# Kernel tuning notes

Measured on AMD Instinct MI355X. Metric: run time of the kernel, lower is better.

The kernel has to match this reference:

```python
import jax, jax.numpy as jnp
import numpy as np

B, S, D = 4, 4096, 2048
DFF = 4 * D
SKIP = 0.125


def setup_inputs() -> dict:
    key = jax.random.key(0)
    ks = jax.random.split(key, 4)
    s_in = 1.0 / np.sqrt(D).astype(np.float32)
    s_ff = 1.0 / np.sqrt(DFF).astype(np.float32)
    return {
        "x": jax.random.normal(ks[0], (B, S, D), jnp.float32),
        "Wr": jax.random.normal(ks[1], (D, 1), jnp.float32) * s_in,
        "br": jnp.zeros((1,), jnp.float32),
        "W1": jax.random.normal(ks[2], (D, DFF), jnp.float32) * s_in,
        "b1": jnp.zeros((DFF,), jnp.float32),
        "W2": jax.random.normal(ks[3], (DFF, D), jnp.float32) * s_ff,
        "b2": jnp.zeros((D,), jnp.float32),
    }


def reference(x, Wr, br, W1, b1, W2, b2):
    Bs, Ss, Ds = x.shape
    k = max(int(Ss * SKIP), 1)
    # Router: tiny linear D -> 1
    logits = (x @ Wr + br)[..., 0]                      # [B, S]
    # Top-k token selection along sequence
    weights, idx = jax.lax.top_k(logits, k)             # [B, k] (unsorted order within topk)
    perm = jnp.argsort(idx, axis=1)                     # torch.sort's sort-indices
    tokens = jnp.take_along_axis(idx, perm, axis=1)     # sorted token positions [B, k]
    # Gather selected tokens
    fx = jnp.take_along_axis(x, tokens[..., None], axis=1)  # [B, k, D]
    h = jax.nn.gelu(fx @ W1 + b1, approximate=False)    # [B, k, 4D]
    out_l = h @ W2 + b2                                  # [B, k, D]
    # Softmax over topk router logits, reordered to sorted-token order
    tw = jax.nn.softmax(weights, axis=1)                # [B, k]
    rw = jnp.take_along_axis(tw, perm, axis=1)          # [B, k]
    xw = rw[..., None] * out_l                           # [B, k, D]
    # scatter_add back onto x at the selected token positions
    bidx = jnp.arange(Bs)[:, None]                       # [B, 1]
    return x.at[bidx, tokens].add(xw)
```

## Files before the change

### kernel.cpp

```cpp
#include <hip/hip_runtime.h>
#include <math.h>

#define B_DIM   4
#define S_DIM   4096
#define D_DIM   2048
#define DFF_DIM 8192
#define K_TOP   512
#define M_ROWS  (B_DIM * K_TOP)
#define NSPLIT  4

typedef _Float16 half8 __attribute__((ext_vector_type(8)));
typedef _Float16 half4 __attribute__((ext_vector_type(4)));
typedef float    floatx4 __attribute__((ext_vector_type(4)));

static const size_t OFF_LOGITS = 0;
static const size_t OFF_SELMAP = 0;
static const size_t OFF_TOK    = 65536;
static const size_t OFF_RW     = 73728;
static const size_t OFF_FX     = 81920;
static const size_t OFF_W1T    = OFF_FX  + (size_t)M_ROWS * D_DIM * 2;
static const size_t OFF_W2T    = OFF_W1T + (size_t)DFF_DIM * D_DIM * 2;
static const size_t OFF_H      = OFF_W2T + (size_t)D_DIM * DFF_DIM * 2;
static const size_t WS_NEEDED  = OFF_H   + (size_t)M_ROWS * DFF_DIM * 2;
static const size_t OFF_PART   = OFF_W1T;

__device__ __forceinline__ void async_ld16(const void* g, void* l) {
  __builtin_amdgcn_global_load_lds((const __attribute__((address_space(1))) unsigned int*)g,
                                   (__attribute__((address_space(3))) unsigned int*)l,
                                   16, 0, 0);
}

#define WAITCNT_VM0   0x0F70
#define WAITCNT_LGKM0 0xC07F

__global__ __launch_bounds__(256) void router_logits(const float* __restrict__ x,
                                                     const float* __restrict__ Wr,
                                                     const float* __restrict__ br,
                                                     float* __restrict__ logits) {
  int row  = blockIdx.x * 4 + (threadIdx.x >> 6);
  int lane = threadIdx.x & 63;
  const float4* xr = (const float4*)(x + (size_t)row * D_DIM);
  const float4* wr = (const float4*)Wr;
  float s = 0.f;
#pragma unroll
  for (int i = 0; i < (D_DIM / 4) / 64; ++i) {
    float4 a = xr[lane + i * 64];
    float4 w = wr[lane + i * 64];
    s += a.x * w.x + a.y * w.y + a.z * w.z + a.w * w.w;
  }
#pragma unroll
  for (int off = 32; off > 0; off >>= 1) s += __shfl_down(s, off, 64);
  if (lane == 0) logits[row] = s + br[0];
}

__global__ __launch_bounds__(256) void topk_select(const float* logits,
                                                   int* selmap,
                                                   int* __restrict__ tokens,
                                                   float* __restrict__ rw) {
  int b = blockIdx.x;
  const float* lg = logits + (size_t)b * S_DIM;
  __shared__ unsigned int keys[S_DIM];
  __shared__ unsigned int bins[256];
  __shared__ unsigned int sscan[256];
  __shared__ unsigned int sh_prefix, sh_r;
  __shared__ float sel_logit[K_TOP];
  __shared__ float red[8];

  int tid = threadIdx.x;
  for (int s = tid; s < S_DIM; s += 256) {
    unsigned int u = __float_as_uint(lg[s]);
    keys[s] = (u & 0x80000000u) ? ~u : (u | 0x80000000u);
    selmap[b * S_DIM + s] = -1;
  }
  if (tid == 0) { sh_prefix = 0u; sh_r = K_TOP; }
  __syncthreads();

  for (int p = 24; p >= 0; p -= 8) {
    bins[tid] = 0u;
    __syncthreads();
    unsigned int prefix = sh_prefix;
    unsigned int maskhi = (p == 24) ? 0u : (0xFFFFFFFFu << (p + 8));
    for (int s = tid; s < S_DIM; s += 256) {
      unsigned int kk = keys[s];
      if ((kk & maskhi) == prefix) atomicAdd(&bins[(kk >> p) & 255u], 1u);
    }
    __syncthreads();
    sscan[tid] = bins[255 - tid];
    __syncthreads();
#pragma unroll
    for (int off = 1; off < 256; off <<= 1) {
      unsigned int v = (tid >= off) ? sscan[tid - off] : 0u;
      __syncthreads();
      sscan[tid] += v;
      __syncthreads();
    }
    unsigned int r = sh_r;
    unsigned int above = (tid > 0) ? sscan[tid - 1] : 0u;
    bool hit = (sscan[tid] >= r) && (above < r);
    __syncthreads();
    if (hit) {
      sh_prefix = prefix | ((unsigned int)(255 - tid) << p);
      sh_r = r - above;
    }
    __syncthreads();
  }
  unsigned int T = sh_prefix;

  int s0 = tid * 16;
  unsigned int g = 0, e = 0;
#pragma unroll
  for (int j = 0; j < 16; ++j) {
    unsigned int kk = keys[s0 + j];
    g += (kk > T);
    e += (kk == T);
  }
  sscan[tid] = g | (e << 16);
  __syncthreads();
#pragma unroll
  for (int off = 1; off < 256; off <<= 1) {
    unsigned int v = (tid >= off) ? sscan[tid - off] : 0u;
    __syncthreads();
    sscan[tid] += v;
    __syncthreads();
  }
  unsigned int incl = sscan[tid];
  unsigned int Gtot = sscan[255] & 0xFFFFu;
  unsigned int need = (unsigned int)K_TOP - Gtot;
  unsigned int gr = (incl & 0xFFFFu) - g;
  unsigned int er = (incl >> 16) - e;
#pragma unroll
  for (int j = 0; j < 16; ++j) {
    unsigned int kk = keys[s0 + j];
    if (kk > T) {
      unsigned int pos = gr + (er < need ? er : need);
      tokens[b * K_TOP + (int)pos] = s0 + j;
      sel_logit[pos] = __uint_as_float((kk & 0x80000000u) ? (kk & 0x7FFFFFFFu) : ~kk);
      selmap[b * S_DIM + s0 + j] = (int)pos;
      gr++;
    } else if (kk == T) {
      if (er < need) {
        unsigned int pos = gr + er;
        tokens[b * K_TOP + (int)pos] = s0 + j;
        sel_logit[pos] = __uint_as_float((kk & 0x80000000u) ? (kk & 0x7FFFFFFFu) : ~kk);
        selmap[b * S_DIM + s0 + j] = (int)pos;
      }
      er++;
    }
  }
  __syncthreads();

  int lane = tid & 63, wv = tid >> 6;
  float mx = -1e30f;
  for (int i = tid; i < K_TOP; i += 256) mx = fmaxf(mx, sel_logit[i]);
#pragma unroll
  for (int off = 32; off > 0; off >>= 1) mx = fmaxf(mx, __shfl_down(mx, off, 64));
  if (lane == 0) red[wv] = mx;
  __syncthreads();
  if (tid == 0) red[0] = fmaxf(fmaxf(red[0], red[1]), fmaxf(red[2], red[3]));
  __syncthreads();
  float M = red[0];
  float sm = 0.f;
  for (int i = tid; i < K_TOP; i += 256) sm += expf(sel_logit[i] - M);
#pragma unroll
  for (int off = 32; off > 0; off >>= 1) sm += __shfl_down(sm, off, 64);
  if (lane == 0) red[4 + wv] = sm;
  __syncthreads();
  if (tid == 0) red[4] = red[4] + red[5] + red[6] + red[7];
  __syncthreads();
  float SUM = red[4];
  for (int i = tid; i < K_TOP; i += 256) rw[b * K_TOP + i] = expf(sel_logit[i] - M) / SUM;
}

__global__ __launch_bounds__(256) void transpose_cvt(const float* __restrict__ in,
                                                     _Float16* __restrict__ out,
                                                     int K, int N) {
  __shared__ float tile[64][65];
  int nb = blockIdx.x * 64, kb = blockIdx.y * 64;
  int tid = threadIdx.x;
  int lr = tid >> 4;
  int lc = (tid & 15) * 4;
#pragma unroll
  for (int p = 0; p < 4; ++p) {
    int row = p * 16 + lr;
    float4 v = *(const float4*)(in + (size_t)(kb + row) * N + nb + lc);
    tile[row][lc] = v.x; tile[row][lc + 1] = v.y; tile[row][lc + 2] = v.z; tile[row][lc + 3] = v.w;
  }
  __syncthreads();
#pragma unroll
  for (int p = 0; p < 2; ++p) {
    int cc = p * 256 + tid;
    int n  = cc >> 3;
    int kc = (cc & 7) * 8;
    half8 o;
#pragma unroll
    for (int j = 0; j < 8; ++j) o[j] = (_Float16)tile[kc + j][n];
    *(half8*)(out + (size_t)(nb + n) * K + kb + kc) = o;
  }
}

__global__ __launch_bounds__(256) void gather_cvt(const float* __restrict__ x,
                                                  const int* __restrict__ tokens,
                                                  _Float16* __restrict__ fx) {
  int row = blockIdx.x;
  int b = row >> 9;
  int token = tokens[row];
  const float4* src = (const float4*)(x + ((size_t)b * S_DIM + token) * D_DIM);
  half4* dst = (half4*)(fx + (size_t)row * D_DIM);
  for (int i = threadIdx.x; i < D_DIM / 4; i += 256) {
    float4 v = src[i];
    half4 o;
    o[0] = (_Float16)v.x; o[1] = (_Float16)v.y; o[2] = (_Float16)v.z; o[3] = (_Float16)v.w;
    dst[i] = o;
  }
}

template <int EPI>
__global__ __launch_bounds__(512, 2) void gemm256(const _Float16* __restrict__ A,
                                                  const _Float16* __restrict__ Bt,
                                                  const float* __restrict__ bias,
                                                  _Float16* __restrict__ Co,
                                                  int M, int N, int K, int Kspan) {
  __shared__ _Float16 As[2][256 * 64];
  __shared__ _Float16 Bs[2][256 * 64];
  const int tid  = threadIdx.x;
  const int lane = tid & 63;
  const int wave = tid >> 6;
  const int wm   = wave >> 2;
  const int wn   = wave & 3;

  const int nwg = gridDim.x * gridDim.y;
  const int bid = blockIdx.y * gridDim.x + blockIdx.x;
  const int swb = (bid & 7) * (nwg >> 3) + (bid >> 3);
  const int bn  = (swb % gridDim.x) * 256;
  const int bm  = (swb / gridDim.x) * 256;

  const int k0 = blockIdx.z * Kspan;
  const int nt = Kspan / 64;

  const int lr  = lane >> 3;
  const int lcs = ((lane & 7) ^ lr) * 8;
  const _Float16* sa[2][2];
  const _Float16* sb[2][2];
  int ldso[2][2];
#pragma unroll
  for (int h = 0; h < 2; ++h)
#pragma unroll
    for (int ci = 0; ci < 2; ++ci) {
      const int cip = 2 * wave + ci;
      const int r   = h * 128 + cip * 8 + lr;
      sa[h][ci] = A  + (size_t)(bm + r) * K + k0 + lcs;
      sb[h][ci] = Bt + (size_t)(bn + r) * K + k0 + lcs;
      ldso[h][ci] = h * 8192 + cip * 512;
    }

  const int mr   = lane & 15;
  const int ksub = lane >> 4;
  const int xr   = mr & 7;
  const int sc0  = (ksub ^ xr) * 8;
  const int sc1  = ((ksub ^ xr) ^ 4) * 8;
  const int aro  = (wm * 128 + mr) * 64;
  const int bro  = (wn * 64 + mr) * 64;

  floatx4 acc[8][4] = {};

#pragma unroll
  for (int h = 0; h < 2; ++h)
#pragma unroll
    for (int ci = 0; ci < 2; ++ci) {
      async_ld16(sa[h][ci], &As[0][ldso[h][ci]]);
      async_ld16(sb[h][ci], &Bs[0][ldso[h][ci]]);
    }
  __builtin_amdgcn_s_waitcnt(WAITCNT_VM0);
  __builtin_amdgcn_s_barrier();

  for (int t = 0; t < nt; ++t) {
    const _Float16* as = As[t & 1];
    const _Float16* bs = Bs[t & 1];
    half8 af[4], bf[4];

#pragma unroll
    for (int i = 0; i < 4; ++i) af[i] = *(const half8*)(as + aro + i * 1024 + sc0);
#pragma unroll
    for (int j = 0; j < 4; ++j) bf[j] = *(const half8*)(bs + bro + j * 1024 + sc0);
    if (t + 1 < nt) {
      const int nb = (t + 1) & 1;
      const int kt = (t + 1) * 64;
#pragma unroll
      for (int h = 0; h < 2; ++h)
#pragma unroll
        for (int ci = 0; ci < 2; ++ci) {
          async_ld16(sa[h][ci] + kt, &As[nb][ldso[h][ci]]);
          async_ld16(sb[h][ci] + kt, &Bs[nb][ldso[h][ci]]);
        }
    }
    __builtin_amdgcn_s_barrier();
    __builtin_amdgcn_s_waitcnt(WAITCNT_LGKM0);
    __builtin_amdgcn_s_setprio(1);
#pragma unroll
    for (int i = 0; i < 4; ++i)
#pragma unroll
      for (int j = 0; j < 4; ++j)
        acc[i][j] = __builtin_amdgcn_mfma_f32_16x16x32_f16(af[i], bf[j], acc[i][j], 0, 0, 0);
    __builtin_amdgcn_s_setprio(0);
    __builtin_amdgcn_s_barrier();

#pragma unroll
    for (int i = 0; i < 4; ++i) af[i] = *(const half8*)(as + aro + 4096 + i * 1024 + sc0);
    __builtin_amdgcn_s_barrier();
    __builtin_amdgcn_s_waitcnt(WAITCNT_LGKM0);
    __builtin_amdgcn_s_setprio(1);
#pragma unroll
    for (int i = 0; i < 4; ++i)
#pragma unroll
      for (int j = 0; j < 4; ++j)
        acc[4 + i][j] = __builtin_amdgcn_mfma_f32_16x16x32_f16(af[i], bf[j], acc[4 + i][j], 0, 0, 0);
    __builtin_amdgcn_s_setprio(0);
    __builtin_amdgcn_s_barrier();

#pragma unroll
    for (int i = 0; i < 4; ++i) af[i] = *(const half8*)(as + aro + i * 1024 + sc1);
#pragma unroll
    for (int j = 0; j < 4; ++j) bf[j] = *(const half8*)(bs + bro + j * 1024 + sc1);
    __builtin_amdgcn_s_barrier();
    __builtin_amdgcn_s_waitcnt(WAITCNT_LGKM0);
    __builtin_amdgcn_s_setprio(1);
#pragma unroll
    for (int i = 0; i < 4; ++i)
#pragma unroll
      for (int j = 0; j < 4; ++j)
        acc[i][j] = __builtin_amdgcn_mfma_f32_16x16x32_f16(af[i], bf[j], acc[i][j], 0, 0, 0);
    __builtin_amdgcn_s_setprio(0);
    __builtin_amdgcn_s_barrier();

#pragma unroll
    for (int i = 0; i < 4; ++i) af[i] = *(const half8*)(as + aro + 4096 + i * 1024 + sc1);
    __builtin_amdgcn_s_barrier();
    __builtin_amdgcn_s_waitcnt(WAITCNT_LGKM0);
    __builtin_amdgcn_s_setprio(1);
#pragma unroll
    for (int i = 0; i < 4; ++i)
#pragma unroll
      for (int j = 0; j < 4; ++j)
        acc[4 + i][j] = __builtin_amdgcn_mfma_f32_16x16x32_f16(af[i], bf[j], acc[4 + i][j], 0, 0, 0);
    __builtin_amdgcn_s_setprio(0);
    __builtin_amdgcn_s_waitcnt(WAITCNT_VM0);
    __builtin_amdgcn_s_barrier();
  }

  const int r0 = (lane >> 4) * 4;
  const int cn = lane & 15;
  if (EPI == 0) {
#pragma unroll
    for (int i = 0; i < 8; ++i) {
      const int row = bm + wm * 128 + (i >> 2) * 64 + (i & 3) * 16 + r0;
#pragma unroll
      for (int j = 0; j < 4; ++j) {
        const int col = bn + wn * 64 + j * 16 + cn;
        const float bv = bias[col];
#pragma unroll
        for (int r = 0; r < 4; ++r) {
          float v = acc[i][j][r] + bv;
          v = 0.5f * v * (1.0f + erff(v * 0.7071067811865475f));
          Co[(size_t)(row + r) * N + col] = (_Float16)v;
        }
      }
    }
  } else {
    const size_t zoff = (size_t)blockIdx.z * M;
#pragma unroll
    for (int i = 0; i < 8; ++i) {
      const int row = bm + wm * 128 + (i >> 2) * 64 + (i & 3) * 16 + r0;
#pragma unroll
      for (int j = 0; j < 4; ++j) {
        const int col = bn + wn * 64 + j * 16 + cn;
#pragma unroll
        for (int r = 0; r < 4; ++r)
          Co[(zoff + row + r) * N + col] = (_Float16)acc[i][j][r];
      }
    }
  }
}

__global__ __launch_bounds__(256) void finalize(const float* __restrict__ x,
                                                const _Float16* __restrict__ part,
                                                const float* __restrict__ bias,
                                                const int* __restrict__ selmap,
                                                const float* __restrict__ rw,
                                                float* __restrict__ out) {
  int row = blockIdx.x;
  size_t base = (size_t)row * D_DIM;
  int sel = selmap[row];
  int c = threadIdx.x * 8;
  float4 o0 = *(const float4*)(x + base + c);
  float4 o1 = *(const float4*)(x + base + c + 4);
  if (sel >= 0) {
    float wgt = rw[sel];
    float acc[8] = {0, 0, 0, 0, 0, 0, 0, 0};
#pragma unroll
    for (int kz = 0; kz < NSPLIT; ++kz) {
      half8 p = *(const half8*)(part + ((size_t)kz * M_ROWS + sel) * D_DIM + c);
#pragma unroll
      for (int j = 0; j < 8; ++j) acc[j] += (float)p[j];
    }
    float4 b0 = *(const float4*)(bias + c);
    float4 b1 = *(const float4*)(bias + c + 4);
    o0.x += wgt * (acc[0] + b0.x);
    o0.y += wgt * (acc[1] + b0.y);
    o0.z += wgt * (acc[2] + b0.z);
    o0.w += wgt * (acc[3] + b0.w);
    o1.x += wgt * (acc[4] + b1.x);
    o1.y += wgt * (acc[5] + b1.y);
    o1.z += wgt * (acc[6] + b1.z);
    o1.w += wgt * (acc[7] + b1.w);
  }
  *(float4*)(out + base + c)     = o0;
  *(float4*)(out + base + c + 4) = o1;
}

extern "C" void kernel_launch(void* const* d_in, const int* in_sizes, int n_in,
                              void* d_out, int out_size, void* d_ws, size_t ws_size,
                              hipStream_t stream) {
  const float* x  = (const float*)d_in[0];
  const float* Wr = (const float*)d_in[1];
  const float* br = (const float*)d_in[2];
  const float* W1 = (const float*)d_in[3];
  const float* b1 = (const float*)d_in[4];
  const float* W2 = (const float*)d_in[5];
  const float* b2 = (const float*)d_in[6];
  float* out = (float*)d_out;

  if (ws_size < WS_NEEDED) return;

  char* ws = (char*)d_ws;
  float*     logits = (float*)(ws + OFF_LOGITS);
  int*       selmap = (int*)(ws + OFF_SELMAP);
  int*       tokens = (int*)(ws + OFF_TOK);
  float*     rw     = (float*)(ws + OFF_RW);
  _Float16*  fx     = (_Float16*)(ws + OFF_FX);
  _Float16*  W1T    = (_Float16*)(ws + OFF_W1T);
  _Float16*  W2T    = (_Float16*)(ws + OFF_W2T);
  _Float16*  h      = (_Float16*)(ws + OFF_H);
  _Float16*  part   = (_Float16*)(ws + OFF_PART);

  transpose_cvt<<<dim3(DFF_DIM / 64, D_DIM / 64), 256, 0, stream>>>(W1, W1T, D_DIM, DFF_DIM);
  transpose_cvt<<<dim3(D_DIM / 64, DFF_DIM / 64), 256, 0, stream>>>(W2, W2T, DFF_DIM, D_DIM);

  router_logits<<<(B_DIM * S_DIM) / 4, 256, 0, stream>>>(x, Wr, br, logits);
  topk_select<<<B_DIM, 256, 0, stream>>>(logits, selmap, tokens, rw);
  gather_cvt<<<M_ROWS, 256, 0, stream>>>(x, tokens, fx);

  gemm256<0><<<dim3(DFF_DIM / 256, M_ROWS / 256, 1), 512, 0, stream>>>(
      fx, W1T, b1, h, M_ROWS, DFF_DIM, D_DIM, D_DIM);
  gemm256<2><<<dim3(D_DIM / 256, M_ROWS / 256, NSPLIT), 512, 0, stream>>>(
      h, W2T, nullptr, part, M_ROWS, D_DIM, DFF_DIM, DFF_DIM / NSPLIT);
  finalize<<<B_DIM * S_DIM, 256, 0, stream>>>(x, part, b2, selmap, rw, out);
}
```

Before: 570.0 us.

## Double-buffer MFMA fragment registers to overlap LDS reads with matrix math

```diff
diff --git a/kernel.cpp b/kernel.cpp
--- a/kernel.cpp
+++ b/kernel.cpp
@@ -31,7 +31,6 @@
 }
 
 #define WAITCNT_VM0   0x0F70
-#define WAITCNT_LGKM0 0xC07F
 
 __global__ __launch_bounds__(256) void router_logits(const float* __restrict__ x,
                                                      const float* __restrict__ Wr,
@@ -214,6 +213,16 @@
   }
 }
 
+#define MFMA_CLUSTER(ACCBASE, AF, BF)                                                   \
+  __builtin_amdgcn_s_setprio(1);                                                        \
+  _Pragma("unroll")                                                                     \
+  for (int i_ = 0; i_ < 4; ++i_)                                                        \
+    _Pragma("unroll")                                                                   \
+    for (int j_ = 0; j_ < 4; ++j_)                                                      \
+      acc[(ACCBASE) + i_][j_] =                                                         \
+          __builtin_amdgcn_mfma_f32_16x16x32_f16(AF[i_], BF[j_], acc[(ACCBASE) + i_][j_], 0, 0, 0); \
+  __builtin_amdgcn_s_setprio(0);
+
 template <int EPI>
 __global__ __launch_bounds__(512, 2) void gemm256(const _Float16* __restrict__ A,
                                                   const _Float16* __restrict__ Bt,
@@ -224,7 +233,7 @@
   __shared__ _Float16 Bs[2][256 * 64];
   const int tid  = threadIdx.x;
   const int lane = tid & 63;
-  const int wave = tid >> 6;
+  const int wave = __builtin_amdgcn_readfirstlane(tid >> 6);
   const int wm   = wave >> 2;
   const int wn   = wave & 3;
 
@@ -239,17 +248,16 @@
 
   const int lr  = lane >> 3;
   const int lcs = ((lane & 7) ^ lr) * 8;
-  const _Float16* sa[2][2];
-  const _Float16* sb[2][2];
-  int ldso[2][2];
+  const _Float16* a_lane = A  + (size_t)(bm + lr) * K + k0 + lcs;
+  const _Float16* b_lane = Bt + (size_t)(bn + lr) * K + k0 + lcs;
+  size_t goff[2][2];
+  int    ldso[2][2];
 #pragma unroll
   for (int h = 0; h < 2; ++h)
 #pragma unroll
     for (int ci = 0; ci < 2; ++ci) {
       const int cip = 2 * wave + ci;
-      const int r   = h * 128 + cip * 8 + lr;
-      sa[h][ci] = A  + (size_t)(bm + r) * K + k0 + lcs;
-      sb[h][ci] = Bt + (size_t)(bn + r) * K + k0 + lcs;
+      goff[h][ci] = (size_t)(h * 128 + cip * 8) * K;
       ldso[h][ci] = h * 8192 + cip * 512;
     }
 
@@ -262,88 +270,72 @@
   const int bro  = (wn * 64 + mr) * 64;
 
   floatx4 acc[8][4] = {};
+  half8 af_a[4], af_b[4], bf_a[4], bf_b[4];
 
 #pragma unroll
   for (int h = 0; h < 2; ++h)
 #pragma unroll
     for (int ci = 0; ci < 2; ++ci) {
-      async_ld16(sa[h][ci], &As[0][ldso[h][ci]]);
-      async_ld16(sb[h][ci], &Bs[0][ldso[h][ci]]);
+      async_ld16(a_lane + goff[h][ci], &As[0][ldso[h][ci]]);
+      async_ld16(b_lane + goff[h][ci], &Bs[0][ldso[h][ci]]);
     }
   __builtin_amdgcn_s_waitcnt(WAITCNT_VM0);
   __builtin_amdgcn_s_barrier();
+  __builtin_amdgcn_sched_barrier(0);
+#pragma unroll
+  for (int i = 0; i < 4; ++i) af_a[i] = *(const half8*)(&As[0][aro + i * 1024 + sc0]);
+#pragma unroll
+  for (int j = 0; j < 4; ++j) bf_a[j] = *(const half8*)(&Bs[0][bro + j * 1024 + sc0]);
 
   for (int t = 0; t < nt; ++t) {
     const _Float16* as = As[t & 1];
     const _Float16* bs = Bs[t & 1];
-    half8 af[4], bf[4];
-
-#pragma unroll
-    for (int i = 0; i < 4; ++i) af[i] = *(const half8*)(as + aro + i * 1024 + sc0);
-#pragma unroll
-    for (int j = 0; j < 4; ++j) bf[j] = *(const half8*)(bs + bro + j * 1024 + sc0);
+
     if (t + 1 < nt) {
-      const int nb = (t + 1) & 1;
       const int kt = (t + 1) * 64;
+      _Float16* an = &As[(t + 1) & 1][0];
+      _Float16* bn2 = &Bs[(t + 1) & 1][0];
 #pragma unroll
       for (int h = 0; h < 2; ++h)
 #pragma unroll
         for (int ci = 0; ci < 2; ++ci) {
-          async_ld16(sa[h][ci] + kt, &As[nb][ldso[h][ci]]);
-          async_ld16(sb[h][ci] + kt, &Bs[nb][ldso[h][ci]]);
+          async_ld16(a_lane + goff[h][ci] + kt, an + ldso[h][ci]);
+          async_ld16(b_lane + goff[h][ci] + kt, bn2 + ldso[h][ci]);
         }
     }
+#pragma unroll
+    for (int i = 0; i < 4; ++i) af_b[i] = *(const half8*)(as + aro + 4096 + i * 1024 + sc0);
+    __builtin_amdgcn_sched_barrier(0);
+    MFMA_CLUSTER(0, af_a, bf_a)
     __builtin_amdgcn_s_barrier();
-    __builtin_amdgcn_s_waitcnt(WAITCNT_LGKM0);
-    __builtin_amdgcn_s_setprio(1);
-#pragma unroll
-    for (int i = 0; i < 4; ++i)
-#pragma unroll
-      for (int j = 0; j < 4; ++j)
-        acc[i][j] = __builtin_amdgcn_mfma_f32_16x16x32_f16(af[i], bf[j], acc[i][j], 0, 0, 0);
-    __builtin_amdgcn_s_setprio(0);
+
+#pragma unroll
+    for (int i = 0; i < 4; ++i) af_a[i] = *(const half8*)(as + aro + i * 1024 + sc1);
+#pragma unroll
+    for (int j = 0; j < 4; ++j) bf_b[j] = *(const half8*)(bs + bro + j * 1024 + sc1);
+    __builtin_amdgcn_sched_barrier(0);
+    MFMA_CLUSTER(4, af_b, bf_a)
     __builtin_amdgcn_s_barrier();
 
 #pragma unroll
-    for (int i = 0; i < 4; ++i) af[i] = *(const half8*)(as + aro + 4096 + i * 1024 + sc0);
+    for (int i = 0; i < 4; ++i) af_b[i] = *(const half8*)(as + aro + 4096 + i * 1024 + sc1);
+    __builtin_amdgcn_sched_barrier(0);
+    MFMA_CLUSTER(0, af_a, bf_b)
     __builtin_amdgcn_s_barrier();
-    __builtin_amdgcn_s_waitcnt(WAITCNT_LGKM0);
-    __builtin_amdgcn_s_setprio(1);
-#pragma unroll
-    for (int i = 0; i < 4; ++i)
-#pragma unroll
-      for (int j = 0; j < 4; ++j)
-        acc[4 + i][j] = __builtin_amdgcn_mfma_f32_16x16x32_f16(af[i], bf[j], acc[4 + i][j], 0, 0, 0);
-    __builtin_amdgcn_s_setprio(0);
+
+    __builtin_amdgcn_s_waitcnt(WAITCNT_VM0);
     __builtin_amdgcn_s_barrier();
-
-#pragma unroll
-    for (int i = 0; i < 4; ++i) af[i] = *(const half8*)(as + aro + i * 1024 + sc1);
-#pragma unroll
-    for (int j = 0; j < 4; ++j) bf[j] = *(const half8*)(bs + bro + j * 1024 + sc1);
-    __builtin_amdgcn_s_barrier();
-    __builtin_amdgcn_s_waitcnt(WAITCNT_LGKM0);
-    __builtin_amdgcn_s_setprio(1);
-#pragma unroll
-    for (int i = 0; i < 4; ++i)
-#pragma unroll
-      for (int j = 0; j < 4; ++j)
-        acc[i][j] = __builtin_amdgcn_mfma_f32_16x16x32_f16(af[i], bf[j], acc[i][j], 0, 0, 0);
-    __builtin_amdgcn_s_setprio(0);
-    __builtin_amdgcn_s_barrier();
-
-#pragma unroll
-    for (int i = 0; i < 4; ++i) af[i] = *(const half8*)(as + aro + 4096 + i * 1024 + sc1);
-    __builtin_amdgcn_s_barrier();
-    __builtin_amdgcn_s_waitcnt(WAITCNT_LGKM0);
-    __builtin_amdgcn_s_setprio(1);
-#pragma unroll
-    for (int i = 0; i < 4; ++i)
-#pragma unroll
-      for (int j = 0; j < 4; ++j)
-        acc[4 + i][j] = __builtin_amdgcn_mfma_f32_16x16x32_f16(af[i], bf[j], acc[4 + i][j], 0, 0, 0);
-    __builtin_amdgcn_s_setprio(0);
-    __builtin_amdgcn_s_waitcnt(WAITCNT_VM0);
+    __builtin_amdgcn_sched_barrier(0);
+    if (t + 1 < nt) {
+      const _Float16* asn = As[(t + 1) & 1];
+      const _Float16* bsn = Bs[(t + 1) & 1];
+#pragma unroll
+      for (int i = 0; i < 4; ++i) af_a[i] = *(const half8*)(asn + aro + i * 1024 + sc0);
+#pragma unroll
+      for (int j = 0; j < 4; ++j) bf_a[j] = *(const half8*)(bsn + bro + j * 1024 + sc0);
+    }
+    __builtin_amdgcn_sched_barrier(0);
+    MFMA_CLUSTER(4, af_b, bf_b)
     __builtin_amdgcn_s_barrier();
   }
 
```

New measurement: 579.8 us. About the same (+1.7%).
